# Optimization experiments

Hardware: AMD Instinct MI355X
Metric: run time of the kernel (lower is better)

Reference implementation:

```python
import jax, jax.numpy as jnp
import numpy as np

N_AB = 8
L = 3
N_REF = 3
ANC = 0
M = 20
NV = N_AB
NQ = N_AB + N_REF + ANC  # 11
K = N_AB - L             # 5
DIM = 2 ** NQ            # 2048

# CNOT as (in_c, in_t, out_c, out_t); matches einsum 'bvf,fg->bvg' with f=(q1,q2) bits
CNOT4 = jnp.array([[1., 0, 0, 0],
                   [0, 1, 0, 0],
                   [0, 0, 0, 1],
                   [0, 0, 1, 0]], dtype=jnp.float32).reshape(2, 2, 2, 2)


def ry_mat(angle):
    c = jnp.cos(angle / 2.0)
    s = jnp.sin(angle / 2.0)
    # [[c, -s], [s, c]]; original contracts as state @ gate ('bvi,ij->bvj')
    return jnp.stack([jnp.stack([c, -s]), jnp.stack([s, c])])


def apply_1q(state, q, gate):
    # state: [b, 2^NQ]; qubit q is big-endian axis q of [2]*NQ view
    b = state.shape[0]
    t = state.reshape(b, 2 ** q, 2, -1)
    out = jnp.einsum('blir,ij->bljr', t, gate)
    return out.reshape(b, -1)


def apply_2q(state, q1, q2, gate4):
    # gate4: [2,2,2,2] with indices (in_q1, in_q2, out_q1, out_q2)
    b = state.shape[0]
    a, c = (q1, q2) if q1 < q2 else (q2, q1)
    t = state.reshape(b, 2 ** a, 2, 2 ** (c - a - 1), 2, -1)
    if q1 < q2:
        out = jnp.einsum('bxiyjz,ijkl->bxkylz', t, gate4)
    else:
        out = jnp.einsum('bxjyiz,ijkl->bxlykz', t, gate4)
    return out.reshape(b, -1)


def setup_inputs() -> dict:
    key = jax.random.key(0)
    k1, k2 = jax.random.split(key)
    x = jax.random.uniform(k1, (1024, 2 ** N_AB), dtype=jnp.float32)
    theta = jax.random.normal(k2, ((M + 1) * NV,), dtype=jnp.float32) * 0.08
    return {"x": x, "theta": theta}


def reference(x, theta):
    b = x.shape[0]
    # amplitude encode: state[:, i << (n_ref+anc)] = x[:, i]
    inds = np.arange(2 ** N_AB) << (N_REF + ANC)
    state = jnp.zeros((b, DIM), dtype=x.dtype).at[:, inds].set(x)
    pidx = 0
    for m in range(M):
        for q in range(NV):
            state = apply_1q(state, q, ry_mat(theta[pidx + q]))
        pidx += NV
        # cw_fixed ring: control q -> target (q+1) % NV
        for q in range(NV):
            state = apply_2q(state, q, (q + 1) % NV, CNOT4)
    for q in range(NV):
        state = apply_1q(state, q, ry_mat(theta[pidx + q]))
    # qubits: A = 0..K-1, B = K..K+L-1, Bp = rest (anc=0)
    t = state.reshape(b, 2 ** K, 2 ** L, 2 ** N_REF)
    probs_B = jnp.sum(t * t, axis=(1, 3))  # [b, 2^L]
    return probs_B
```

## Files before the change

### kernel.cpp

```cpp
#include <hip/hip_runtime.h>


namespace {

struct M8 { unsigned r[8]; };

constexpr M8 kI{{0x01,0x02,0x04,0x08,0x10,0x20,0x40,0x80}};
constexpr M8 kP{{0xFF,0xFE,0xFC,0xF8,0xF0,0xE0,0xC0,0x7F}};
constexpr M8 kQ{{0x03,0x06,0x0C,0x18,0x30,0x60,0xC1,0x81}};

constexpr M8 mul(const M8& A, const M8& B) {
  M8 C{{0,0,0,0,0,0,0,0}};
  for (int j = 0; j < 8; ++j) {
    unsigned by = 0;
    for (int b = 0; b < 8; ++b) by |= ((B.r[b] >> j) & 1u) << b;
    for (int b = 0; b < 8; ++b) {
      unsigned v = A.r[b] & by;
      v ^= v >> 4; v ^= v >> 2; v ^= v >> 1;
      C.r[b] |= (v & 1u) << j;
    }
  }
  return C;
}

constexpr bool eqI(const M8& A) {
  bool e = true;
  for (int b = 0; b < 8; ++b) e = e && (A.r[b] == (1u << b));
  return e;
}

struct Tables { unsigned Mm[21][8]; unsigned Rr[21][8]; bool ok; };

constexpr Tables build() {
  Tables t{};
  M8 T = kI, Ti = kI;
  bool ok = eqI(mul(kP, kQ)) && eqI(mul(kQ, kP));
  for (int m = 0; m <= 20; ++m) {
    ok = ok && eqI(mul(T, Ti));
    for (int b = 0; b < 8; ++b) {
      unsigned mm = 0;
      for (int k = 0; k < 8; ++k) mm |= ((Ti.r[k] >> b) & 1u) << k;
      t.Mm[m][b] = mm;
      t.Rr[m][b] = T.r[b];
    }
    T = mul(kP, T);
    Ti = mul(Ti, kQ);
  }
  t.ok = ok;
  return t;
}

constexpr Tables kT = build();
static_assert(kT.ok, "GF(2) inverse tracking failed");
static_assert(kT.Mm[0][5] == 0x20 && kT.Rr[0][3] == 0x08, "layer-0 must be identity");

template<unsigned M, int J>
__device__ __forceinline__ float part(const float (&s)[4]) {
  constexpr int jj = J ^ (int)(M & 3u);
  constexpr int lm = (int)(M >> 2);
  float v = s[jj];
  if constexpr (lm != 0) v = __shfl_xor(v, lm);
  return v;
}

template<int m, int st>
__device__ __forceinline__ void stage(int lane, const float4* __restrict__ ct4, float (&s)[4]) {
  constexpr int bA = 2 * st + 1, bB = 2 * st;
  constexpr unsigned MA = kT.Mm[m][bA];
  constexpr unsigned MB = kT.Mm[m][bB];
  constexpr unsigned MC = MA ^ MB;
  constexpr unsigned RA = kT.Rr[m][bA];
  constexpr unsigned RB = kT.Rr[m][bB];

  const float4 k = ct4[m * 4 + st];
  const int sa = (__popc((int)(RA >> 2) & lane) & 1) << 31;
  const int sb = (__popc((int)(RB >> 2) & lane) & 1) << 31;

  float A[4] = { part<MA,0>(s), part<MA,1>(s), part<MA,2>(s), part<MA,3>(s) };
  float B[4] = { part<MB,0>(s), part<MB,1>(s), part<MB,2>(s), part<MB,3>(s) };
  float C[4] = { part<MC,0>(s), part<MC,1>(s), part<MC,2>(s), part<MC,3>(s) };

  float ns[4];
  #pragma unroll
  for (int j = 0; j < 4; ++j) {
    const int ka = ((__popc((int)(RA & 3u) & j) & 1) << 31) ^ sa;
    const int kb = ((__popc((int)(RB & 3u) & j) & 1) << 31) ^ sb;
    const float wa = __int_as_float(__float_as_int(k.y) ^ ka);
    const float wb = __int_as_float(__float_as_int(k.z) ^ kb);
    const float wc = __int_as_float(__float_as_int(k.w) ^ ka ^ kb);
    ns[j] = k.x * s[j] + wa * A[j] + wb * B[j] + wc * C[j];
  }
  s[0] = ns[0]; s[1] = ns[1]; s[2] = ns[2]; s[3] = ns[3];
}

template<int m>
__device__ __forceinline__ void run_layers(int lane, const float4* __restrict__ ct4, float (&s)[4]) {
  if constexpr (m <= 20) {
    stage<m, 0>(lane, ct4, s);
    stage<m, 1>(lane, ct4, s);
    stage<m, 2>(lane, ct4, s);
    stage<m, 3>(lane, ct4, s);
    run_layers<m + 1>(lane, ct4, s);
  }
}

}

__global__ __launch_bounds__(256) void qae_kernel(const float* __restrict__ x,
                                                  const float* __restrict__ theta,
                                                  float* __restrict__ out) {
  __shared__ float4 ct4[84];
  const int t = threadIdx.x;
  if (t < 84) {
    const int m = t >> 2, st = t & 3;
    const int qa = 6 - 2 * st;
    const int qb = 7 - 2 * st;
    float sA, cA, sB, cB;
    sincosf(theta[m * 8 + qa] * 0.5f, &sA, &cA);
    sincosf(theta[m * 8 + qb] * 0.5f, &sB, &cB);
    ct4[t] = make_float4(cA * cB, sA * cB, cA * sB, sA * sB);
  }
  __syncthreads();

  const int lane = t & 63;
  const int b = blockIdx.x * 4 + (t >> 6);

  const float4 xv = *reinterpret_cast<const float4*>(x + (size_t)b * 256 + lane * 4);
  float s[4] = { xv.x, xv.y, xv.z, xv.w };

  run_layers<0>(lane, ct4, s);

  constexpr unsigned R0 = kT.Rr[20][0], R1 = kT.Rr[20][1], R2 = kT.Rr[20][2];
  const int q0 = __popc((int)(R0 >> 2) & lane) & 1;
  const int q1 = __popc((int)(R1 >> 2) & lane) & 1;
  const int q2 = __popc((int)(R2 >> 2) & lane) & 1;

  float acc[8];
  #pragma unroll
  for (int B = 0; B < 8; ++B) acc[B] = 0.f;
  #pragma unroll
  for (int j = 0; j < 4; ++j) {
    const int bj = (q0 ^ (__popc((int)(R0 & 3u) & j) & 1))
                 | ((q1 ^ (__popc((int)(R1 & 3u) & j) & 1)) << 1)
                 | ((q2 ^ (__popc((int)(R2 & 3u) & j) & 1)) << 2);
    const float pj = s[j] * s[j];
    #pragma unroll
    for (int B = 0; B < 8; ++B) acc[B] += (bj == B) ? pj : 0.f;
  }
  #pragma unroll
  for (int mm = 1; mm < 64; mm <<= 1) {
    #pragma unroll
    for (int B = 0; B < 8; ++B) acc[B] += __shfl_xor(acc[B], mm);
  }
  if (lane == 0) {
    float4* o = reinterpret_cast<float4*>(out + (size_t)b * 8);
    o[0] = make_float4(acc[0], acc[1], acc[2], acc[3]);
    o[1] = make_float4(acc[4], acc[5], acc[6], acc[7]);
  }
}

extern "C" void kernel_launch(void* const* d_in, const int* in_sizes, int n_in,
                              void* d_out, int out_size, void* d_ws, size_t ws_size,
                              hipStream_t stream) {
  const float* x = (const float*)d_in[0];
  const float* theta = (const float*)d_in[1];
  float* out = (float*)d_out;
  qae_kernel<<<256, 256, 0, stream>>>(x, theta, out);
}
```

Before: 21.14 us.

## Search per-layer gate pairing at compile time and process two batch rows per wave

Replaces the fixed adjacent-qubit pairing of rotation gates with a compile-time search that picks, for each layer, the grouping of qubits into pairs or singles that needs the fewest cross-lane shuffles. Each wave now evolves two batch rows at once, with blocks halved to 128 threads, so each coefficient load and sign computation is shared and there is more independent work to hide shuffle latency. The cost is more registers per thread and fewer waves in total (512 instead of 1024) for the GPU to spread across its compute units.

```diff
diff --git a/kernel.cpp b/kernel.cpp
--- a/kernel.cpp
+++ b/kernel.cpp
@@ -52,110 +52,269 @@
 
 constexpr Tables kT = build();
 static_assert(kT.ok, "GF(2) inverse tracking failed");
-static_assert(kT.Mm[0][5] == 0x20 && kT.Rr[0][3] == 0x08, "layer-0 must be identity");
-
-template<unsigned M, int J>
-__device__ __forceinline__ float part(const float (&s)[4]) {
-  constexpr int jj = J ^ (int)(M & 3u);
-  constexpr int lm = (int)(M >> 2);
-  float v = s[jj];
-  if constexpr (lm != 0) v = __shfl_xor(v, lm);
-  return v;
-}
-
-template<int m, int st>
-__device__ __forceinline__ void stage(int lane, const float4* __restrict__ ct4, float (&s)[4]) {
-  constexpr int bA = 2 * st + 1, bB = 2 * st;
-  constexpr unsigned MA = kT.Mm[m][bA];
-  constexpr unsigned MB = kT.Mm[m][bB];
-  constexpr unsigned MC = MA ^ MB;
-  constexpr unsigned RA = kT.Rr[m][bA];
-  constexpr unsigned RB = kT.Rr[m][bB];
-
-  const float4 k = ct4[m * 4 + st];
-  const int sa = (__popc((int)(RA >> 2) & lane) & 1) << 31;
-  const int sb = (__popc((int)(RB >> 2) & lane) & 1) << 31;
-
-  float A[4] = { part<MA,0>(s), part<MA,1>(s), part<MA,2>(s), part<MA,3>(s) };
-  float B[4] = { part<MB,0>(s), part<MB,1>(s), part<MB,2>(s), part<MB,3>(s) };
-  float C[4] = { part<MC,0>(s), part<MC,1>(s), part<MC,2>(s), part<MC,3>(s) };
-
-  float ns[4];
-  #pragma unroll
-  for (int j = 0; j < 4; ++j) {
-    const int ka = ((__popc((int)(RA & 3u) & j) & 1) << 31) ^ sa;
-    const int kb = ((__popc((int)(RB & 3u) & j) & 1) << 31) ^ sb;
-    const float wa = __int_as_float(__float_as_int(k.y) ^ ka);
-    const float wb = __int_as_float(__float_as_int(k.z) ^ kb);
-    const float wc = __int_as_float(__float_as_int(k.w) ^ ka ^ kb);
-    ns[j] = k.x * s[j] + wa * A[j] + wb * B[j] + wc * C[j];
-  }
-  s[0] = ns[0]; s[1] = ns[1]; s[2] = ns[2]; s[3] = ns[3];
+
+constexpr int single_cost(int m, int a) {
+  return (((kT.Mm[m][a] >> 2) != 0) ? 8 : 0) + 1;
+}
+constexpr int pair_cost(int m, int a, int b) {
+  const unsigned LA = kT.Mm[m][a] >> 2, LB = kT.Mm[m][b] >> 2, LC = LA ^ LB;
+  int c = 0;
+  if (LA) ++c;
+  if (LB && LB != LA) ++c;
+  if (LC && LC != LA && LC != LB) ++c;
+  return 8 * c + 1;
+}
+
+struct PlanCost { int n; int pa[8]; int pb[8]; int cost; };
+
+constexpr PlanCost search(int m, unsigned used) {
+  if (used == 0xFFu) {
+    PlanCost r{0, {0,0,0,0,0,0,0,0}, {0,0,0,0,0,0,0,0}, 0};
+    return r;
+  }
+  int a = 0;
+  while ((used >> a) & 1u) ++a;
+  PlanCost best = search(m, used | (1u << a));
+  best.pa[best.n] = a; best.pb[best.n] = -1;
+  best.n += 1; best.cost += single_cost(m, a);
+  for (int b = a + 1; b < 8; ++b) {
+    if ((used >> b) & 1u) continue;
+    PlanCost sub = search(m, used | (1u << a) | (1u << b));
+    const int c = sub.cost + pair_cost(m, a, b);
+    if (c < best.cost) {
+      sub.pa[sub.n] = a; sub.pb[sub.n] = b;
+      sub.n += 1; sub.cost = c;
+      best = sub;
+    }
+  }
+  return best;
+}
+
+struct AllPlans { int nops[21]; int pa[21][8]; int pb[21][8]; };
+
+constexpr AllPlans build_plans() {
+  AllPlans ap{};
+  for (int m = 0; m < 21; ++m) {
+    const PlanCost pc = search(m, 0u);
+    ap.nops[m] = pc.n;
+    for (int k = 0; k < 8; ++k) {
+      ap.pa[m][k] = (k < pc.n) ? pc.pa[k] : 0;
+      ap.pb[m][k] = (k < pc.n) ? pc.pb[k] : -1;
+    }
+  }
+  return ap;
+}
+
+constexpr AllPlans kPlans = build_plans();
+
+constexpr bool plans_ok() {
+  for (int m = 0; m < 21; ++m) {
+    unsigned mask = 0; int cnt = 0;
+    for (int k = 0; k < kPlans.nops[m]; ++k) {
+      mask |= 1u << kPlans.pa[m][k]; ++cnt;
+      if (kPlans.pb[m][k] >= 0) { mask |= 1u << kPlans.pb[m][k]; ++cnt; }
+    }
+    if (mask != 0xFFu || cnt != 8) return false;
+  }
+  return true;
+}
+static_assert(plans_ok(), "bad gate schedule");
+
+__constant__ AllPlans dPlans = build_plans();
+
+struct LaneSet { unsigned L[3]; };
+constexpr LaneSet lane_set(unsigned a, unsigned b, unsigned c) {
+  LaneSet r{{0,0,0}}; int n = 0;
+  const unsigned v[3] = {a, b, c};
+  for (int i = 0; i < 3; ++i) {
+    if (!v[i]) continue;
+    bool dup = false;
+    for (int j = 0; j < n; ++j) if (r.L[j] == v[i]) dup = true;
+    if (!dup) r.L[n++] = v[i];
+  }
+  return r;
+}
+
+template<unsigned RX, int IDX>
+__device__ __forceinline__ float pick(const float (&s)[4], const float (&t0)[4],
+                                      const float (&t1)[4], const float (&t2)[4], int j) {
+  if constexpr (IDX == 0) return t0[j ^ (int)RX];
+  else if constexpr (IDX == 1) return t1[j ^ (int)RX];
+  else if constexpr (IDX == 2) return t2[j ^ (int)RX];
+  else return s[j ^ (int)RX];
+}
+
+template<int m, int op>
+__device__ __forceinline__ void do_op(int lane, const float4* __restrict__ ct4,
+                                      float (&s)[4], float (&u)[4]) {
+  constexpr int ga = kPlans.pa[m][op];
+  constexpr int gb = kPlans.pb[m][op];
+  constexpr unsigned MA = kT.Mm[m][ga];
+  constexpr unsigned RA = kT.Rr[m][ga];
+  constexpr unsigned LA = MA >> 2;
+  const float4 k = ct4[m * 8 + op];
+
+  if constexpr (gb < 0) {
+    float tAs[4], tAu[4];
+    #pragma unroll
+    for (int j = 0; j < 4; ++j) {
+      float ps = s[j ^ (int)(MA & 3u)];
+      float pu = u[j ^ (int)(MA & 3u)];
+      if constexpr (LA != 0) { ps = __shfl_xor(ps, (int)LA); pu = __shfl_xor(pu, (int)LA); }
+      tAs[j] = ps; tAu[j] = pu;
+    }
+    const int sa = __popc((int)(RA >> 2) & lane) & 1;
+    const float wa = sa ? -k.y : k.y;
+    float ns[4], nu[4];
+    #pragma unroll
+    for (int j = 0; j < 4; ++j) {
+      const int pj = __popc((int)(RA & 3u) & j) & 1;
+      const float va = pj ? -wa : wa;
+      ns[j] = fmaf(va, tAs[j], k.x * s[j]);
+      nu[j] = fmaf(va, tAu[j], k.x * u[j]);
+    }
+    #pragma unroll
+    for (int j = 0; j < 4; ++j) { s[j] = ns[j]; u[j] = nu[j]; }
+  } else {
+    constexpr unsigned MB = kT.Mm[m][gb], MC = MA ^ MB;
+    constexpr unsigned RB = kT.Rr[m][gb];
+    constexpr unsigned LB = MB >> 2, LC = MC >> 2;
+    constexpr LaneSet LS = lane_set(LA, LB, LC);
+    constexpr unsigned L1 = LS.L[0], L2 = LS.L[1], L3 = LS.L[2];
+    constexpr int iA = (LA == 0) ? -1 : (LA == L1 ? 0 : (LA == L2 ? 1 : 2));
+    constexpr int iB = (LB == 0) ? -1 : (LB == L1 ? 0 : (LB == L2 ? 1 : 2));
+    constexpr int iC = (LC == 0) ? -1 : (LC == L1 ? 0 : (LC == L2 ? 1 : 2));
+
+    float b1s[4], b1u[4], b2s[4], b2u[4], b3s[4], b3u[4];
+    if constexpr (L1 != 0) {
+      #pragma unroll
+      for (int j = 0; j < 4; ++j) { b1s[j] = __shfl_xor(s[j], (int)L1); b1u[j] = __shfl_xor(u[j], (int)L1); }
+    }
+    if constexpr (L2 != 0) {
+      #pragma unroll
+      for (int j = 0; j < 4; ++j) { b2s[j] = __shfl_xor(s[j], (int)L2); b2u[j] = __shfl_xor(u[j], (int)L2); }
+    }
+    if constexpr (L3 != 0) {
+      #pragma unroll
+      for (int j = 0; j < 4; ++j) { b3s[j] = __shfl_xor(s[j], (int)L3); b3u[j] = __shfl_xor(u[j], (int)L3); }
+    }
+
+    const int sa = __popc((int)(RA >> 2) & lane) & 1;
+    const int sb = __popc((int)(RB >> 2) & lane) & 1;
+    const float wa = sa ? -k.y : k.y;
+    const float wb = sb ? -k.z : k.z;
+    const float wc = (sa ^ sb) ? -k.w : k.w;
+
+    float ns[4], nu[4];
+    #pragma unroll
+    for (int j = 0; j < 4; ++j) {
+      const int pa_ = __popc((int)(RA & 3u) & j) & 1;
+      const int pb_ = __popc((int)(RB & 3u) & j) & 1;
+      const float vA = pa_ ? -wa : wa;
+      const float vB = pb_ ? -wb : wb;
+      const float vC = (pa_ ^ pb_) ? -wc : wc;
+      ns[j] = fmaf(vC, pick<MC & 3u, iC>(s, b1s, b2s, b3s, j),
+              fmaf(vB, pick<MB & 3u, iB>(s, b1s, b2s, b3s, j),
+              fmaf(vA, pick<MA & 3u, iA>(s, b1s, b2s, b3s, j), k.x * s[j])));
+      nu[j] = fmaf(vC, pick<MC & 3u, iC>(u, b1u, b2u, b3u, j),
+              fmaf(vB, pick<MB & 3u, iB>(u, b1u, b2u, b3u, j),
+              fmaf(vA, pick<MA & 3u, iA>(u, b1u, b2u, b3u, j), k.x * u[j])));
+    }
+    #pragma unroll
+    for (int j = 0; j < 4; ++j) { s[j] = ns[j]; u[j] = nu[j]; }
+  }
+}
+
+template<int m, int op>
+__device__ __forceinline__ void run_ops(int lane, const float4* __restrict__ ct4,
+                                        float (&s)[4], float (&u)[4]) {
+  if constexpr (op < kPlans.nops[m]) {
+    do_op<m, op>(lane, ct4, s, u);
+    run_ops<m, op + 1>(lane, ct4, s, u);
+  }
 }
 
 template<int m>
-__device__ __forceinline__ void run_layers(int lane, const float4* __restrict__ ct4, float (&s)[4]) {
+__device__ __forceinline__ void run_all(int lane, const float4* __restrict__ ct4,
+                                        float (&s)[4], float (&u)[4]) {
   if constexpr (m <= 20) {
-    stage<m, 0>(lane, ct4, s);
-    stage<m, 1>(lane, ct4, s);
-    stage<m, 2>(lane, ct4, s);
-    stage<m, 3>(lane, ct4, s);
-    run_layers<m + 1>(lane, ct4, s);
-  }
-}
-
-}
-
-__global__ __launch_bounds__(256) void qae_kernel(const float* __restrict__ x,
+    run_ops<m, 0>(lane, ct4, s, u);
+    run_all<m + 1>(lane, ct4, s, u);
+  }
+}
+
+}
+
+__global__ __launch_bounds__(128) void qae_kernel(const float* __restrict__ x,
                                                   const float* __restrict__ theta,
                                                   float* __restrict__ out) {
-  __shared__ float4 ct4[84];
+  __shared__ float4 ct4[168];
   const int t = threadIdx.x;
-  if (t < 84) {
-    const int m = t >> 2, st = t & 3;
-    const int qa = 6 - 2 * st;
-    const int qb = 7 - 2 * st;
-    float sA, cA, sB, cB;
-    sincosf(theta[m * 8 + qa] * 0.5f, &sA, &cA);
-    sincosf(theta[m * 8 + qb] * 0.5f, &sB, &cB);
-    ct4[t] = make_float4(cA * cB, sA * cB, cA * sB, sA * sB);
+  for (int tt = t; tt < 168; tt += 128) {
+    const int m = tt >> 3, op = tt & 7;
+    if (op < dPlans.nops[m]) {
+      const int ga = dPlans.pa[m][op], gb = dPlans.pb[m][op];
+      float sA, cA;
+      sincosf(theta[m * 8 + (7 - ga)] * 0.5f, &sA, &cA);
+      if (gb >= 0) {
+        float sB, cB;
+        sincosf(theta[m * 8 + (7 - gb)] * 0.5f, &sB, &cB);
+        ct4[tt] = make_float4(cA * cB, sA * cB, cA * sB, sA * sB);
+      } else {
+        ct4[tt] = make_float4(cA, sA, 0.f, 0.f);
+      }
+    }
   }
   __syncthreads();
 
   const int lane = t & 63;
-  const int b = blockIdx.x * 4 + (t >> 6);
-
-  const float4 xv = *reinterpret_cast<const float4*>(x + (size_t)b * 256 + lane * 4);
-  float s[4] = { xv.x, xv.y, xv.z, xv.w };
-
-  run_layers<0>(lane, ct4, s);
+  const int wave = t >> 6;
+  const int b0 = blockIdx.x * 4 + wave * 2;
+
+  const float4 xv0 = *reinterpret_cast<const float4*>(x + (size_t)b0 * 256 + lane * 4);
+  const float4 xv1 = *reinterpret_cast<const float4*>(x + (size_t)(b0 + 1) * 256 + lane * 4);
+  float s[4] = {xv0.x, xv0.y, xv0.z, xv0.w};
+  float u[4] = {xv1.x, xv1.y, xv1.z, xv1.w};
+
+  run_all<0>(lane, ct4, s, u);
 
   constexpr unsigned R0 = kT.Rr[20][0], R1 = kT.Rr[20][1], R2 = kT.Rr[20][2];
   const int q0 = __popc((int)(R0 >> 2) & lane) & 1;
   const int q1 = __popc((int)(R1 >> 2) & lane) & 1;
   const int q2 = __popc((int)(R2 >> 2) & lane) & 1;
 
-  float acc[8];
+  float accS[8], accU[8];
   #pragma unroll
-  for (int B = 0; B < 8; ++B) acc[B] = 0.f;
+  for (int B = 0; B < 8; ++B) { accS[B] = 0.f; accU[B] = 0.f; }
   #pragma unroll
   for (int j = 0; j < 4; ++j) {
     const int bj = (q0 ^ (__popc((int)(R0 & 3u) & j) & 1))
                  | ((q1 ^ (__popc((int)(R1 & 3u) & j) & 1)) << 1)
                  | ((q2 ^ (__popc((int)(R2 & 3u) & j) & 1)) << 2);
-    const float pj = s[j] * s[j];
-    #pragma unroll
-    for (int B = 0; B < 8; ++B) acc[B] += (bj == B) ? pj : 0.f;
+    const float ps = s[j] * s[j];
+    const float pu = u[j] * u[j];
+    #pragma unroll
+    for (int B = 0; B < 8; ++B) {
+      accS[B] += (bj == B) ? ps : 0.f;
+      accU[B] += (bj == B) ? pu : 0.f;
+    }
   }
   #pragma unroll
   for (int mm = 1; mm < 64; mm <<= 1) {
     #pragma unroll
-    for (int B = 0; B < 8; ++B) acc[B] += __shfl_xor(acc[B], mm);
+    for (int B = 0; B < 8; ++B) {
+      accS[B] += __shfl_xor(accS[B], mm);
+      accU[B] += __shfl_xor(accU[B], mm);
+    }
   }
   if (lane == 0) {
-    float4* o = reinterpret_cast<float4*>(out + (size_t)b * 8);
-    o[0] = make_float4(acc[0], acc[1], acc[2], acc[3]);
-    o[1] = make_float4(acc[4], acc[5], acc[6], acc[7]);
+    float4* o = reinterpret_cast<float4*>(out + (size_t)b0 * 8);
+    o[0] = make_float4(accS[0], accS[1], accS[2], accS[3]);
+    o[1] = make_float4(accS[4], accS[5], accS[6], accS[7]);
+  } else if (lane == 1) {
+    float4* o = reinterpret_cast<float4*>(out + (size_t)(b0 + 1) * 8);
+    o[0] = make_float4(accU[0], accU[1], accU[2], accU[3]);
+    o[1] = make_float4(accU[4], accU[5], accU[6], accU[7]);
   }
 }
 
@@ -165,5 +324,5 @@
   const float* x = (const float*)d_in[0];
   const float* theta = (const float*)d_in[1];
   float* out = (float*)d_out;
-  qae_kernel<<<256, 256, 0, stream>>>(x, theta, out);
-}
+  qae_kernel<<<256, 128, 0, stream>>>(x, theta, out);
+}
```

Measured after the change: 22.57 us. 1.07x slower.
